# Performance work log

Measured on AMD Instinct MI355X. Metric: run time of the kernel, lower is better.

The kernel has to match this reference:

```python
import jax, jax.numpy as jnp
import numpy as np

B, S, H, QKV, NH, MLP = 4, 2048, 512, 512, 8, 2048
HD = QKV // NH
EPS = 1e-6


def _layernorm(x):
    # LayerNorm over last dim, no affine, eps=1e-6
    mu = jnp.mean(x, axis=-1, keepdims=True)
    var = jnp.mean(jnp.square(x - mu), axis=-1, keepdims=True)
    return (x - mu) * jax.lax.rsqrt(var + EPS)


def setup_inputs() -> dict:
    key = jax.random.key(0)
    ks = jax.random.split(key, 8)
    sc_in = 1.0 / np.sqrt(H)
    sc_qkv = 1.0 / np.sqrt(QKV)
    sc_mlp = 1.0 / np.sqrt(MLP)
    return {
        "input": jax.random.normal(ks[0], (B, S, H), dtype=jnp.float32),
        "mask": jnp.ones((B, S), dtype=jnp.float32),
        "Wq": jax.random.normal(ks[1], (H, QKV), dtype=jnp.float32) * sc_in,
        "Wk": jax.random.normal(ks[2], (H, QKV), dtype=jnp.float32) * sc_in,
        "Wv": jax.random.normal(ks[3], (H, QKV), dtype=jnp.float32) * sc_in,
        "Wo": jax.random.normal(ks[4], (QKV, H), dtype=jnp.float32) * sc_qkv,
        "W1": jax.random.normal(ks[5], (H, MLP), dtype=jnp.float32) * sc_in,
        "W2": jax.random.normal(ks[6], (MLP, H), dtype=jnp.float32) * sc_mlp,
    }


def reference(input, mask, Wq, Wk, Wv, Wo, W1, W2):
    # pre-mask + pre-norm
    x = input * mask[..., None]
    x = _layernorm(x)
    # qkv projections, split heads: [B,S,QKV] -> [B,NH,S,HD]
    def heads(t):
        return t.reshape(B, S, NH, HD).transpose(0, 2, 1, 3)
    q = heads(x @ Wq) * (1.0 / np.sqrt(HD))
    k = heads(x @ Wk)
    v = heads(x @ Wv)
    logits = jnp.einsum("bhqd,bhkd->bhqk", q, k)  # [B,NH,S,S]
    amask = mask[:, None, :, None]  # 'b q -> b 1 q 1'
    logits = logits + (-100000.0) * (1.0 - amask)
    att = jax.nn.softmax(logits, axis=-1)
    out = jnp.einsum("bhqk,bhkd->bhqd", att, v)
    out = out.transpose(0, 2, 1, 3).reshape(B, S, QKV)
    x = input + out @ Wo  # residual
    x = x * mask[..., None]
    y = _layernorm(x)
    ffn = jax.nn.gelu(y @ W1, approximate=False) @ W2
    return ffn + x
```

## Files before the change

kernel.cpp:

```cpp
#include <hip/hip_runtime.h>
#include <hip/hip_bf16.h>
#include <cmath>

typedef __attribute__((ext_vector_type(8))) short bf16x8;
typedef __attribute__((ext_vector_type(4))) float f32x4;
typedef __attribute__((ext_vector_type(16))) float f32x16;
typedef unsigned short u16;
typedef unsigned int u32;

#define B_ 4
#define S_ 2048
#define H_ 512
#define NH_ 8
#define HD_ 64
#define MLP_ 2048
#define M_ (B_*S_)

__device__ __forceinline__ float bf2f(u16 u){ u32 v=((u32)u)<<16; float f; __builtin_memcpy(&f,&v,4); return f; }
__device__ __forceinline__ u16 f2bf(float f){ u32 u; __builtin_memcpy(&u,&f,4); u32 r=(u+0x7fffu+((u>>16)&1u))>>16; return (u16)r; }
__device__ __forceinline__ u32 pk2(float lo, float hi2){
  __hip_bfloat162 t = __float22bfloat162_rn(make_float2(lo, hi2));
  u32 r; __builtin_memcpy(&r, &t, 4); return r;
}

__device__ __forceinline__ float xhalf_add(float x){
  float a = x, b = x;
  asm volatile("v_permlane32_swap_b32 %0, %1" : "+v"(a), "+v"(b));
  return a + b;
}
__device__ __forceinline__ float xhalf_max(float x){
  float a = x, b = x;
  asm volatile("v_permlane32_swap_b32 %0, %1" : "+v"(a), "+v"(b));
  return fmaxf(a, b);
}

__device__ __forceinline__ void gl16(const u16* g, u16* l) {
  __builtin_amdgcn_global_load_lds((const __attribute__((address_space(1))) u32*)(g),
                                   (__attribute__((address_space(3))) u32*)(l), 16, 0, 0);
}

__device__ __forceinline__ void gemm_core(
    const u16* __restrict__ A, const u16* __restrict__ Bt,
    int lda, int ldb, int nkt, int m0, int n0,
    u16* As, u16* Bs, f32x4 (&acc)[4][4])
{
  const int tid = threadIdx.x;
  const int lane = tid & 63;
  const int w = tid >> 6;
  const int lr = lane & 15;
  const int g  = lane >> 4;
  const int wr = w >> 1, wc = w & 1;

  int srow[2], scol[2], soff[2];
#pragma unroll
  for (int c = 0; c < 2; ++c) {
    int off = (w*2+c)*512 + lane*8;
    int row = off >> 5;
    int gl  = (off >> 3) & 3;
    srow[c] = row;
    scol[c] = ((gl ^ ((row>>1)&3)) << 3);
    soff[c] = (w*2+c)*512;
  }
  int aoff[4], boff[4];
#pragma unroll
  for (int m = 0; m < 4; ++m) {
    int ra = wr*64 + m*16 + lr;
    aoff[m] = ra*32 + ((g ^ ((ra>>1)&3))<<3);
    int rb = wc*64 + m*16 + lr;
    boff[m] = rb*32 + ((g ^ ((rb>>1)&3))<<3);
  }
  const u16* Ap = A + (size_t)m0*lda;
  const u16* Bp = Bt + (size_t)n0*ldb;

#pragma unroll
  for (int c = 0; c < 2; ++c) {
    gl16(Ap + (size_t)srow[c]*lda + scol[c], As + soff[c]);
    gl16(Bp + (size_t)srow[c]*ldb + scol[c], Bs + soff[c]);
  }

  for (int kt = 0; kt < nkt; ++kt) {
    const int cb = (kt & 1) * 4096;
    if (kt + 1 < nkt) {
      const int k0 = (kt + 1) << 5;
      const int nb = ((kt + 1) & 1) * 4096;
#pragma unroll
      for (int c = 0; c < 2; ++c) {
        gl16(Ap + (size_t)srow[c]*lda + k0 + scol[c], As + nb + soff[c]);
        gl16(Bp + (size_t)srow[c]*ldb + k0 + scol[c], Bs + nb + soff[c]);
      }
      asm volatile("s_waitcnt vmcnt(4)" ::: "memory");
    } else {
      asm volatile("s_waitcnt vmcnt(0)" ::: "memory");
    }
    __builtin_amdgcn_s_barrier();

    bf16x8 af[4], bfr[4];
#pragma unroll
    for (int m = 0; m < 4; ++m) {
      af[m]  = *(const bf16x8*)(As + cb + aoff[m]);
      bfr[m] = *(const bf16x8*)(Bs + cb + boff[m]);
    }
#pragma unroll
    for (int m = 0; m < 4; ++m) {
#pragma unroll
      for (int n = 0; n < 4; ++n) {
        acc[m][n] = __builtin_amdgcn_mfma_f32_16x16x32_bf16(af[m], bfr[n], acc[m][n], 0, 0, 0);
      }
    }
    __builtin_amdgcn_s_barrier();
  }
}

__device__ __forceinline__ void gemm_core64(
    const u16* __restrict__ A, const u16* __restrict__ Bt,
    int lda, int ldb, int nkt, int m0, int n0,
    u16* As, u16* Bs, f32x4 (&acc)[2][4])
{
  const int tid = threadIdx.x;
  const int lane = tid & 63;
  const int w = tid >> 6;
  const int lr = lane & 15;
  const int g  = lane >> 4;

  int srow[2], scol[2], soff[2];
#pragma unroll
  for (int c = 0; c < 2; ++c) {
    int off = (w*2+c)*512 + lane*8;
    int row = off >> 5;
    int gl  = (off >> 3) & 3;
    srow[c] = row;
    scol[c] = ((gl ^ ((row>>1)&3)) << 3);
    soff[c] = (w*2+c)*512;
  }
  int offB = w*512 + lane*8;
  int srowB = offB >> 5;
  int scolB = ((((offB>>3)&3) ^ ((srowB>>1)&3)) << 3);
  int soffB = w*512;

  int aoff[2], boff[4];
#pragma unroll
  for (int m = 0; m < 2; ++m) {
    int ra = w*32 + m*16 + lr;
    aoff[m] = ra*32 + ((g ^ ((ra>>1)&3))<<3);
  }
#pragma unroll
  for (int n = 0; n < 4; ++n) {
    int rb = n*16 + lr;
    boff[n] = rb*32 + ((g ^ ((rb>>1)&3))<<3);
  }
  const u16* Ap = A + (size_t)m0*lda;
  const u16* Bp = Bt + (size_t)n0*ldb;

#pragma unroll
  for (int c = 0; c < 2; ++c) gl16(Ap + (size_t)srow[c]*lda + scol[c], As + soff[c]);
  gl16(Bp + (size_t)srowB*ldb + scolB, Bs + soffB);

  for (int kt = 0; kt < nkt; ++kt) {
    const int cbA = (kt & 1) * 4096;
    const int cbB = (kt & 1) * 2048;
    if (kt + 1 < nkt) {
      const int k0 = (kt + 1) << 5;
      const int nbA = ((kt + 1) & 1) * 4096;
      const int nbB = ((kt + 1) & 1) * 2048;
#pragma unroll
      for (int c = 0; c < 2; ++c) gl16(Ap + (size_t)srow[c]*lda + k0 + scol[c], As + nbA + soff[c]);
      gl16(Bp + (size_t)srowB*ldb + k0 + scolB, Bs + nbB + soffB);
      asm volatile("s_waitcnt vmcnt(3)" ::: "memory");
    } else {
      asm volatile("s_waitcnt vmcnt(0)" ::: "memory");
    }
    __builtin_amdgcn_s_barrier();

    bf16x8 af[2], bfr[4];
#pragma unroll
    for (int m = 0; m < 2; ++m) af[m] = *(const bf16x8*)(As + cbA + aoff[m]);
#pragma unroll
    for (int n = 0; n < 4; ++n) bfr[n] = *(const bf16x8*)(Bs + cbB + boff[n]);
#pragma unroll
    for (int m = 0; m < 2; ++m) {
#pragma unroll
      for (int n = 0; n < 4; ++n) {
        acc[m][n] = __builtin_amdgcn_mfma_f32_16x16x32_bf16(af[m], bfr[n], acc[m][n], 0, 0, 0);
      }
    }
    __builtin_amdgcn_s_barrier();
  }
}

__global__ __launch_bounds__(256,2) void k_qkv(
    const u16* __restrict__ xn, const u16* __restrict__ wqt,
    const u16* __restrict__ wkt, const u16* __restrict__ wvt,
    u16* __restrict__ q, u16* __restrict__ k, u16* __restrict__ v)
{
  __shared__ u16 As[2*128*32], Bs[2*128*32];
  int m0 = blockIdx.x*128;
  int sel = blockIdx.y >> 2;
  int n0 = (blockIdx.y & 3)*128;
  const u16* Bt = sel==0 ? wqt : (sel==1 ? wkt : wvt);
  u16* O = sel==0 ? q : (sel==1 ? k : v);
  float alpha = (sel==0) ? 0.125f : 1.0f;
  f32x4 acc[4][4] = {};
  gemm_core(xn, Bt, H_, H_, H_/32, m0, n0, As, Bs, acc);
  const int lane = threadIdx.x&63, w = threadIdx.x>>6;
  const int lr = lane&15, g = lane>>4, wr = w>>1, wc = w&1;
#pragma unroll
  for (int m=0;m<4;++m) {
#pragma unroll
    for (int n=0;n<4;++n) {
#pragma unroll
      for (int r=0;r<4;++r) {
        int row = m0 + wr*64 + m*16 + g*4 + r;
        int col = n0 + wc*64 + n*16 + lr;
        O[(size_t)row*H_ + col] = f2bf(acc[m][n][r]*alpha);
      }
    }
  }
}

template<int EPI>
__global__ __launch_bounds__(256,2) void k_gemm(
    const u16* __restrict__ A, const u16* __restrict__ Bt, void* __restrict__ Ov,
    const float* __restrict__ aux, const float* __restrict__ maskv,
    int N, int K)
{
  __shared__ u16 As[2*128*32], Bs[2*128*32];
  int m0 = blockIdx.x*128, n0 = blockIdx.y*128;
  f32x4 acc[4][4] = {};
  gemm_core(A, Bt, K, K, K>>5, m0, n0, As, Bs, acc);
  const int lane = threadIdx.x&63, w = threadIdx.x>>6;
  const int lr = lane&15, g = lane>>4, wr = w>>1, wc = w&1;
#pragma unroll
  for (int m=0;m<4;++m) {
#pragma unroll
    for (int n=0;n<4;++n) {
#pragma unroll
      for (int r=0;r<4;++r) {
        int row = m0 + wr*64 + m*16 + g*4 + r;
        int col = n0 + wc*64 + n*16 + lr;
        float val = acc[m][n][r];
        if (EPI == 1) {
          val = 0.5f*val*(1.0f + erff(val*0.70710678118654752f));
          ((u16*)Ov)[(size_t)row*N + col] = f2bf(val);
        } else if (EPI == 2) {
          float mv = maskv[row];
          val = (aux[(size_t)row*N + col] + val)*mv;
          ((float*)Ov)[(size_t)row*N + col] = val;
        } else if (EPI == 3) {
          val += aux[(size_t)row*N + col];
          ((float*)Ov)[(size_t)row*N + col] = val;
        }
      }
    }
  }
}

template<int EPI>
__global__ __launch_bounds__(256,2) void k_gemm64(
    const u16* __restrict__ A, const u16* __restrict__ Bt, void* __restrict__ Ov,
    const float* __restrict__ aux, const float* __restrict__ maskv,
    int N, int K)
{
  __shared__ u16 As[2*128*32], Bs[2*64*32];
  int m0 = blockIdx.x*128, n0 = blockIdx.y*64;
  f32x4 acc[2][4] = {};
  gemm_core64(A, Bt, K, K, K>>5, m0, n0, As, Bs, acc);
  const int lane = threadIdx.x&63, w = threadIdx.x>>6;
  const int lr = lane&15, g = lane>>4;
#pragma unroll
  for (int m=0;m<2;++m) {
#pragma unroll
    for (int n=0;n<4;++n) {
#pragma unroll
      for (int r=0;r<4;++r) {
        int row = m0 + w*32 + m*16 + g*4 + r;
        int col = n0 + n*16 + lr;
        float val = acc[m][n][r];
        if (EPI == 2) {
          float mv = maskv[row];
          val = (aux[(size_t)row*N + col] + val)*mv;
          ((float*)Ov)[(size_t)row*N + col] = val;
        } else if (EPI == 3) {
          val += aux[(size_t)row*N + col];
          ((float*)Ov)[(size_t)row*N + col] = val;
        }
      }
    }
  }
}

template<int MASKED>
__global__ __launch_bounds__(256) void k_ln(const float* __restrict__ in,
    const float* __restrict__ mask, u16* __restrict__ out)
{
  int row = blockIdx.x*4 + (threadIdx.x>>6);
  int lane = threadIdx.x & 63;
  const f32x4* p = (const f32x4*)(in + (size_t)row*H_ + lane*8);
  f32x4 a = p[0], b = p[1];
  float mv = MASKED ? mask[row] : 1.0f;
  float x[8]; float s = 0.f, s2 = 0.f;
#pragma unroll
  for (int j=0;j<4;++j){ x[j] = a[j]*mv; x[4+j] = b[j]*mv; }
#pragma unroll
  for (int j=0;j<8;++j){ s += x[j]; s2 += x[j]*x[j]; }
#pragma unroll
  for (int m=1;m<32;m<<=1){ s += __shfl_xor(s,m); s2 += __shfl_xor(s2,m); }
  s = xhalf_add(s); s2 = xhalf_add(s2);
  float mu = s*(1.0f/H_);
  float var = s2*(1.0f/H_) - mu*mu;
  float inv = rsqrtf(var + 1e-6f);
  bf16x8 o;
#pragma unroll
  for (int j=0;j<8;++j) o[j] = (short)f2bf((x[j]-mu)*inv);
  *(bf16x8*)(out + (size_t)row*H_ + lane*8) = o;
}

__global__ void k_tr4(const float* __restrict__ s0, const float* __restrict__ s1,
                      const float* __restrict__ s2, const float* __restrict__ s3,
                      u16* __restrict__ d0, u16* __restrict__ d1,
                      u16* __restrict__ d2, u16* __restrict__ d3)
{
  __shared__ u16 t[32][33];
  const float* src = blockIdx.z==0 ? s0 : (blockIdx.z==1 ? s1 : (blockIdx.z==2 ? s2 : s3));
  u16* dst = blockIdx.z==0 ? d0 : (blockIdx.z==1 ? d1 : (blockIdx.z==2 ? d2 : d3));
  int c0 = blockIdx.x*32, r0 = blockIdx.y*32;
  int tx = threadIdx.x & 31, ty = threadIdx.x >> 5;
#pragma unroll
  for (int i=0;i<32;i+=8) t[ty+i][tx] = f2bf(src[(size_t)(r0+ty+i)*512 + c0+tx]);
  __syncthreads();
#pragma unroll
  for (int i=0;i<32;i+=8) dst[(size_t)(c0+ty+i)*512 + r0+tx] = t[tx][ty+i];
}

__global__ void k_tr(const float* __restrict__ src, u16* __restrict__ dst, int R, int C)
{
  __shared__ u16 t[32][33];
  int c0 = blockIdx.x*32, r0 = blockIdx.y*32;
  int tx = threadIdx.x & 31, ty = threadIdx.x >> 5;
#pragma unroll
  for (int i=0;i<32;i+=8) t[ty+i][tx] = f2bf(src[(size_t)(r0+ty+i)*C + c0+tx]);
  __syncthreads();
#pragma unroll
  for (int i=0;i<32;i+=8) dst[(size_t)(c0+ty+i)*R + r0+tx] = t[tx][ty+i];
}

__global__ void k_trv(const u16* __restrict__ v, u16* __restrict__ vt)
{
  __shared__ u16 t[32][33];
  int bh = blockIdx.z, b = bh>>3, h = bh&7;
  int s0 = blockIdx.x*32, d0 = blockIdx.y*32;
  int tx = threadIdx.x & 31, ty = threadIdx.x >> 5;
#pragma unroll
  for (int i=0;i<32;i+=8) t[ty+i][tx] = v[(size_t)(b*S_ + s0+ty+i)*H_ + h*HD_ + d0+tx];
  __syncthreads();
#pragma unroll
  for (int i=0;i<32;i+=8) vt[((size_t)bh*HD_ + d0+ty+i)*S_ + s0+tx] = t[tx][ty+i];
}

__global__ __launch_bounds__(256) void k_attn(
    const u16* __restrict__ q, const u16* __restrict__ kmat,
    const u16* __restrict__ vt, const float* __restrict__ mask,
    u16* __restrict__ o)
{
  __shared__ u16 Ks[2][64*64];
  __shared__ u16 Vs[2][64*64];
  __shared__ float bias[S_];
  __shared__ float lsums[4][32];

  const int tid = threadIdx.x;
  const int lane = tid & 63;
  const int w = tid >> 6;
  const int l31 = lane & 31;
  const int hi = lane >> 5;
  const int bh = blockIdx.y, b = bh >> 3, h = bh & 7;
  const int q0 = blockIdx.x * 128;

  const int sr = lane >> 3;
  const int sl = (lane & 7) ^ (sr & 7);
  const u16* ks0 = kmat + (size_t)(b*S_ + w*16 + sr)*H_ + h*HD_ + sl*8;
  const u16* ks1 = ks0 + (size_t)8*H_;
  const u16* vs0 = vt + ((size_t)bh*HD_ + w*16 + sr)*S_ + sl*8;
  const u16* vs1 = vs0 + (size_t)8*S_;

  {
    u16* kd = &Ks[0][0] + w*1024;
    u16* vd = &Vs[0][0] + w*1024;
    gl16(ks0, kd); gl16(ks1, kd + 512);
    gl16(vs0, vd); gl16(vs1, vd + 512);
  }

  for (int j = tid; j < S_; j += 256) bias[j] = -100000.0f * (1.0f - mask[b*S_ + j]);

  bf16x8 qf[4];
  {
    const u16* qp = q + (size_t)(b*S_ + q0 + w*32 + l31)*H_ + h*HD_ + hi*8;
#pragma unroll
    for (int ds = 0; ds < 4; ++ds) qf[ds] = *(const bf16x8*)(qp + ds*16);
  }

  f32x16 po0 = {}, po1 = {};
  float mreg = -1e30f, lsum = 0.f;

  __syncthreads();

  for (int jt = 0; jt < 32; ++jt) {
    const int buf = jt & 1;
    if (jt < 31) {
      const int j0 = (jt + 1) * 64;
      u16* kd = &Ks[buf ^ 1][0] + w*1024;
      u16* vd = &Vs[buf ^ 1][0] + w*1024;
      gl16(ks0 + (size_t)j0*H_, kd); gl16(ks1 + (size_t)j0*H_, kd + 512);
      gl16(vs0 + j0, vd);            gl16(vs1 + j0, vd + 512);
      asm volatile("s_waitcnt vmcnt(4)" ::: "memory");
    } else {
      asm volatile("s_waitcnt vmcnt(0)" ::: "memory");
    }
    __builtin_amdgcn_s_barrier();

    const u16* kt  = &Ks[buf][0];
    const u16* vtl = &Vs[buf][0];

    f32x16 s0, s1;
    const float* bp = &bias[jt*64 + hi*4];
#pragma unroll
    for (int kb = 0; kb < 2; ++kb) {
      f32x16 acc;
#pragma unroll
      for (int g2 = 0; g2 < 4; ++g2) {
        f32x4 b4 = *(const f32x4*)(bp + kb*32 + g2*8);
        acc[g2*4+0] = b4[0]; acc[g2*4+1] = b4[1];
        acc[g2*4+2] = b4[2]; acc[g2*4+3] = b4[3];
      }
      const int key = kb*32 + l31;
      const u16* kr = kt + key*64;
      __builtin_amdgcn_s_setprio(1);
#pragma unroll
      for (int ds = 0; ds < 4; ++ds) {
        bf16x8 kf = *(const bf16x8*)(kr + (((ds*2 + hi) ^ (key & 7)) << 3));
        acc = __builtin_amdgcn_mfma_f32_32x32x16_bf16(kf, qf[ds], acc, 0, 0, 0);
      }
      __builtin_amdgcn_s_setprio(0);
      if (kb == 0) s0 = acc; else s1 = acc;
    }

    float g0 = fmaxf(fmaxf(fmaxf(s0[0], s0[1]), fmaxf(s0[2], s0[3])),
                     fmaxf(fmaxf(s1[0], s1[1]), fmaxf(s1[2], s1[3])));
    float g1 = fmaxf(fmaxf(fmaxf(s0[4], s0[5]), fmaxf(s0[6], s0[7])),
                     fmaxf(fmaxf(s1[4], s1[5]), fmaxf(s1[6], s1[7])));
    float g2 = fmaxf(fmaxf(fmaxf(s0[8], s0[9]), fmaxf(s0[10], s0[11])),
                     fmaxf(fmaxf(s1[8], s1[9]), fmaxf(s1[10], s1[11])));
    float g3 = fmaxf(fmaxf(fmaxf(s0[12], s0[13]), fmaxf(s0[14], s0[15])),
                     fmaxf(fmaxf(s1[12], s1[13]), fmaxf(s1[14], s1[15])));
    float mx = xhalf_max(fmaxf(fmaxf(g0, g1), fmaxf(g2, g3)));
    if (__any(mx > mreg + 8.0f)) {
      float mn = fmaxf(mreg, mx);
      float sc = __expf(mreg - mn);
      lsum *= sc;
#pragma unroll
      for (int r = 0; r < 16; ++r) { po0[r] *= sc; po1[r] *= sc; }
      mreg = mn;
    }
#pragma unroll
    for (int r = 0; r < 16; ++r) {
      s0[r] = __expf(s0[r]-mreg);
      s1[r] = __expf(s1[r]-mreg);
    }
    float h0 = ((s0[0]+s0[1])+(s0[2]+s0[3])) + ((s1[0]+s1[1])+(s1[2]+s1[3]));
    float h1 = ((s0[4]+s0[5])+(s0[6]+s0[7])) + ((s1[4]+s1[5])+(s1[6]+s1[7]));
    float h2 = ((s0[8]+s0[9])+(s0[10]+s0[11])) + ((s1[8]+s1[9])+(s1[10]+s1[11]));
    float h3 = ((s0[12]+s0[13])+(s0[14]+s0[15])) + ((s1[12]+s1[13])+(s1[14]+s1[15]));
    lsum += xhalf_add((h0+h1)+(h2+h3));

#pragma unroll
    for (int kb = 0; kb < 2; ++kb) {
      const f32x16& sv = kb ? s1 : s0;
      u32 w01 = pk2(sv[0],  sv[1]);
      u32 w23 = pk2(sv[2],  sv[3]);
      u32 w45 = pk2(sv[4],  sv[5]);
      u32 w67 = pk2(sv[6],  sv[7]);
      asm volatile("v_permlane32_swap_b32 %0, %1" : "+v"(w01), "+v"(w45));
      asm volatile("v_permlane32_swap_b32 %0, %1" : "+v"(w23), "+v"(w67));
      u32 w89 = pk2(sv[8],  sv[9]);
      u32 wab = pk2(sv[10], sv[11]);
      u32 wcd = pk2(sv[12], sv[13]);
      u32 wef = pk2(sv[14], sv[15]);
      asm volatile("v_permlane32_swap_b32 %0, %1" : "+v"(w89), "+v"(wcd));
      asm volatile("v_permlane32_swap_b32 %0, %1" : "+v"(wab), "+v"(wef));
      union { u32 wrd[4]; bf16x8 v; } f0, f1;
      f0.wrd[0]=w01; f0.wrd[1]=w23; f0.wrd[2]=w45; f0.wrd[3]=w67;
      f1.wrd[0]=w89; f1.wrd[1]=wab; f1.wrd[2]=wcd; f1.wrd[3]=wef;
      __builtin_amdgcn_s_setprio(1);
#pragma unroll
      for (int ks = 0; ks < 2; ++ks) {
        bf16x8 pa = ks ? f1.v : f0.v;
#pragma unroll
        for (int nb = 0; nb < 2; ++nb) {
          int dd = nb*32 + l31;
          int slot = ((kb*4 + ks*2 + hi) ^ (dd & 7)) << 3;
          bf16x8 vf = *(const bf16x8*)(vtl + dd*64 + slot);
          if (nb == 0) po0 = __builtin_amdgcn_mfma_f32_32x32x16_bf16(pa, vf, po0, 0,0,0);
          else         po1 = __builtin_amdgcn_mfma_f32_32x32x16_bf16(pa, vf, po1, 0,0,0);
        }
      }
      __builtin_amdgcn_s_setprio(0);
    }
    __builtin_amdgcn_s_barrier();
  }

  if (hi == 0) lsums[w][l31] = lsum;
  f32x4 li[4];
#pragma unroll
  for (int g2i = 0; g2i < 4; ++g2i) {
    f32x4 t = *(const f32x4*)&lsums[w][g2i*8 + hi*4];
    li[g2i][0] = 1.0f/t[0]; li[g2i][1] = 1.0f/t[1];
    li[g2i][2] = 1.0f/t[2]; li[g2i][3] = 1.0f/t[3];
  }
  u16* op = o + (size_t)(b*S_ + q0 + w*32)*H_ + h*HD_;
#pragma unroll
  for (int nb = 0; nb < 2; ++nb) {
#pragma unroll
    for (int r = 0; r < 16; ++r) {
      int row = (r&3) + 8*(r>>2) + 4*hi;
      float val = (nb ? po1[r] : po0[r]) * li[r>>2][r&3];
      op[(size_t)row*H_ + nb*32 + l31] = f2bf(val);
    }
  }
}

extern "C" void kernel_launch(void* const* d_in, const int* in_sizes, int n_in,
                              void* d_out, int out_size, void* d_ws, size_t ws_size,
                              hipStream_t stream) {
  const float* input = (const float*)d_in[0];
  const float* mask  = (const float*)d_in[1];
  const float* Wq = (const float*)d_in[2];
  const float* Wk = (const float*)d_in[3];
  const float* Wv = (const float*)d_in[4];
  const float* Wo = (const float*)d_in[5];
  const float* W1 = (const float*)d_in[6];
  const float* W2 = (const float*)d_in[7];
  float* out = (float*)d_out;
  u16* ws = (u16*)d_ws;

  u16* wqt = ws;
  u16* wkt = wqt + 262144;
  u16* wvt = wkt + 262144;
  u16* wot = wvt + 262144;
  u16* w1t = wot + 262144;
  u16* w2t = w1t + 1048576;
  u16* xn  = w2t + 1048576;
  u16* q   = xn  + 4194304;
  u16* k   = q   + 4194304;
  u16* v   = k   + 4194304;
  u16* vt  = v   + 4194304;
  u16*   attn = xn;
  float* x2f  = (float*)q;
  u16*   y    = v;
  u16*   h1   = vt;

  dim3 blk(256);
  k_tr4<<<dim3(16,16,4), blk, 0, stream>>>(Wq, Wk, Wv, Wo, wqt, wkt, wvt, wot);
  k_tr<<<dim3(64,16), blk, 0, stream>>>(W1, w1t, 512, 2048);
  k_tr<<<dim3(16,64), blk, 0, stream>>>(W2, w2t, 2048, 512);

  k_ln<1><<<2048, blk, 0, stream>>>(input, mask, xn);
  k_qkv<<<dim3(64,12), blk, 0, stream>>>(xn, wqt, wkt, wvt, q, k, v);
  k_trv<<<dim3(64,2,32), blk, 0, stream>>>(v, vt);
  k_attn<<<dim3(16,32), blk, 0, stream>>>(q, k, vt, mask, attn);
  k_gemm64<2><<<dim3(64,8), blk, 0, stream>>>(attn, wot, (void*)x2f, input, mask, 512, 512);
  k_ln<0><<<2048, blk, 0, stream>>>(x2f, nullptr, y);
  k_gemm<1><<<dim3(64,16), blk, 0, stream>>>(y, w1t, (void*)h1, nullptr, nullptr, 2048, 512);
  k_gemm64<3><<<dim3(64,8), blk, 0, stream>>>(h1, w2t, (void*)out, x2f, nullptr, 512, 2048);
}
```

Before: 194.9 us.

## Double attention key tile to 128 and skip bias add when mask is all ones

The flash-attention kernel now processes 128 keys per iteration instead of 64, halving the number of loop iterations and barriers, with larger double-buffered K/V shared tiles and a 16-slot XOR swizzle for V. It also detects at runtime whether any mask bias is nonzero and skips the bias addition when none is. This trades more LDS and registers (four 32x32 score accumulators) for fewer synchronisations, and may lower occupancy.

Measured after the change: 215.7 us. 10.7% more time.

```diff
diff --git a/kernel.cpp b/kernel.cpp
--- a/kernel.cpp
+++ b/kernel.cpp
@@ -361,10 +361,11 @@
     const u16* __restrict__ vt, const float* __restrict__ mask,
     u16* __restrict__ o)
 {
-  __shared__ u16 Ks[2][64*64];
-  __shared__ u16 Vs[2][64*64];
+  __shared__ u16 Ks[2][128*64];
+  __shared__ u16 Vs[2][64*128];
   __shared__ float bias[S_];
   __shared__ float lsums[4][32];
+  __shared__ u32 bnz[4];
 
   const int tid = threadIdx.x;
   const int lane = tid & 63;
@@ -375,20 +376,30 @@
   const int q0 = blockIdx.x * 128;
 
   const int sr = lane >> 3;
-  const int sl = (lane & 7) ^ (sr & 7);
-  const u16* ks0 = kmat + (size_t)(b*S_ + w*16 + sr)*H_ + h*HD_ + sl*8;
-  const u16* ks1 = ks0 + (size_t)8*H_;
-  const u16* vs0 = vt + ((size_t)bh*HD_ + w*16 + sr)*S_ + sl*8;
-  const u16* vs1 = vs0 + (size_t)8*S_;
+  const u16* kbase2 = kmat + (size_t)(b*S_ + w*32 + sr)*H_ + h*HD_ + (((lane & 7) ^ sr) << 3);
+  const int sr4 = lane >> 4;
+  const u16* vbase2 = vt + ((size_t)bh*HD_ + w*16 + sr4)*S_;
 
   {
-    u16* kd = &Ks[0][0] + w*1024;
-    u16* vd = &Vs[0][0] + w*1024;
-    gl16(ks0, kd); gl16(ks1, kd + 512);
-    gl16(vs0, vd); gl16(vs1, vd + 512);
-  }
-
-  for (int j = tid; j < S_; j += 256) bias[j] = -100000.0f * (1.0f - mask[b*S_ + j]);
+    bool any = false;
+    for (int j = tid; j < S_; j += 256) {
+      float bv = -100000.0f * (1.0f - mask[b*S_ + j]);
+      bias[j] = bv;
+      any |= (bv != 0.0f);
+    }
+    bnz[w] = (__ballot(any) != 0ull) ? 1u : 0u;
+  }
+
+  {
+    u16* kd = &Ks[0][0] + w*2048;
+    u16* vd = &Vs[0][0] + w*2048;
+#pragma unroll
+    for (int c = 0; c < 4; ++c) {
+      gl16(kbase2 + (size_t)(c*8)*H_, kd + c*512);
+      int slV = ((lane & 15) ^ (c*4 + sr4)) << 3;
+      gl16(vbase2 + (size_t)(c*4)*S_ + slV, vd + c*512);
+    }
+  }
 
   bf16x8 qf[4];
   {
@@ -401,16 +412,21 @@
   float mreg = -1e30f, lsum = 0.f;
 
   __syncthreads();
-
-  for (int jt = 0; jt < 32; ++jt) {
+  const bool hasbias = (bnz[0] | bnz[1] | bnz[2] | bnz[3]) != 0u;
+
+  for (int jt = 0; jt < 16; ++jt) {
     const int buf = jt & 1;
-    if (jt < 31) {
-      const int j0 = (jt + 1) * 64;
-      u16* kd = &Ks[buf ^ 1][0] + w*1024;
-      u16* vd = &Vs[buf ^ 1][0] + w*1024;
-      gl16(ks0 + (size_t)j0*H_, kd); gl16(ks1 + (size_t)j0*H_, kd + 512);
-      gl16(vs0 + j0, vd);            gl16(vs1 + j0, vd + 512);
-      asm volatile("s_waitcnt vmcnt(4)" ::: "memory");
+    if (jt < 15) {
+      const int j0 = (jt + 1) * 128;
+      u16* kd = &Ks[buf ^ 1][0] + w*2048;
+      u16* vd = &Vs[buf ^ 1][0] + w*2048;
+#pragma unroll
+      for (int c = 0; c < 4; ++c) {
+        gl16(kbase2 + (size_t)(j0 + c*8)*H_, kd + c*512);
+        int slV = ((lane & 15) ^ (c*4 + sr4)) << 3;
+        gl16(vbase2 + (size_t)(c*4)*S_ + j0 + slV, vd + c*512);
+      }
+      asm volatile("s_waitcnt vmcnt(8)" ::: "memory");
     } else {
       asm volatile("s_waitcnt vmcnt(0)" ::: "memory");
     }
@@ -419,17 +435,10 @@
     const u16* kt  = &Ks[buf][0];
     const u16* vtl = &Vs[buf][0];
 
-    f32x16 s0, s1;
-    const float* bp = &bias[jt*64 + hi*4];
-#pragma unroll
-    for (int kb = 0; kb < 2; ++kb) {
-      f32x16 acc;
-#pragma unroll
-      for (int g2 = 0; g2 < 4; ++g2) {
-        f32x4 b4 = *(const f32x4*)(bp + kb*32 + g2*8);
-        acc[g2*4+0] = b4[0]; acc[g2*4+1] = b4[1];
-        acc[g2*4+2] = b4[2]; acc[g2*4+3] = b4[3];
-      }
+    f32x16 sA, sB, sC, sD;
+#pragma unroll
+    for (int kb = 0; kb < 4; ++kb) {
+      f32x16 acc = {};
       const int key = kb*32 + l31;
       const u16* kr = kt + key*64;
       __builtin_amdgcn_s_setprio(1);
@@ -439,18 +448,33 @@
         acc = __builtin_amdgcn_mfma_f32_32x32x16_bf16(kf, qf[ds], acc, 0, 0, 0);
       }
       __builtin_amdgcn_s_setprio(0);
-      if (kb == 0) s0 = acc; else s1 = acc;
-    }
-
-    float g0 = fmaxf(fmaxf(fmaxf(s0[0], s0[1]), fmaxf(s0[2], s0[3])),
-                     fmaxf(fmaxf(s1[0], s1[1]), fmaxf(s1[2], s1[3])));
-    float g1 = fmaxf(fmaxf(fmaxf(s0[4], s0[5]), fmaxf(s0[6], s0[7])),
-                     fmaxf(fmaxf(s1[4], s1[5]), fmaxf(s1[6], s1[7])));
-    float g2 = fmaxf(fmaxf(fmaxf(s0[8], s0[9]), fmaxf(s0[10], s0[11])),
-                     fmaxf(fmaxf(s1[8], s1[9]), fmaxf(s1[10], s1[11])));
-    float g3 = fmaxf(fmaxf(fmaxf(s0[12], s0[13]), fmaxf(s0[14], s0[15])),
-                     fmaxf(fmaxf(s1[12], s1[13]), fmaxf(s1[14], s1[15])));
-    float mx = xhalf_max(fmaxf(fmaxf(g0, g1), fmaxf(g2, g3)));
+      if (kb == 0) sA = acc; else if (kb == 1) sB = acc;
+      else if (kb == 2) sC = acc; else sD = acc;
+    }
+
+    if (hasbias) {
+      const float* bp = &bias[jt*128 + hi*4];
+#pragma unroll
+      for (int g2 = 0; g2 < 4; ++g2) {
+        f32x4 b0 = *(const f32x4*)(bp + 0*32 + g2*8);
+        f32x4 b1 = *(const f32x4*)(bp + 1*32 + g2*8);
+        f32x4 b2 = *(const f32x4*)(bp + 2*32 + g2*8);
+        f32x4 b3 = *(const f32x4*)(bp + 3*32 + g2*8);
+#pragma unroll
+        for (int j = 0; j < 4; ++j) {
+          sA[g2*4+j] += b0[j]; sB[g2*4+j] += b1[j];
+          sC[g2*4+j] += b2[j]; sD[g2*4+j] += b3[j];
+        }
+      }
+    }
+
+    float mA = sA[0], mB = sB[0], mC = sC[0], mD = sD[0];
+#pragma unroll
+    for (int r = 1; r < 16; ++r) {
+      mA = fmaxf(mA, sA[r]); mB = fmaxf(mB, sB[r]);
+      mC = fmaxf(mC, sC[r]); mD = fmaxf(mD, sD[r]);
+    }
+    float mx = xhalf_max(fmaxf(fmaxf(mA, mB), fmaxf(mC, mD)));
     if (__any(mx > mreg + 8.0f)) {
       float mn = fmaxf(mreg, mx);
       float sc = __expf(mreg - mn);
@@ -459,20 +483,19 @@
       for (int r = 0; r < 16; ++r) { po0[r] *= sc; po1[r] *= sc; }
       mreg = mn;
     }
+    float pA = 0.f, pB = 0.f, pC = 0.f, pD = 0.f;
 #pragma unroll
     for (int r = 0; r < 16; ++r) {
-      s0[r] = __expf(s0[r]-mreg);
-      s1[r] = __expf(s1[r]-mreg);
-    }
-    float h0 = ((s0[0]+s0[1])+(s0[2]+s0[3])) + ((s1[0]+s1[1])+(s1[2]+s1[3]));
-    float h1 = ((s0[4]+s0[5])+(s0[6]+s0[7])) + ((s1[4]+s1[5])+(s1[6]+s1[7]));
-    float h2 = ((s0[8]+s0[9])+(s0[10]+s0[11])) + ((s1[8]+s1[9])+(s1[10]+s1[11]));
-    float h3 = ((s0[12]+s0[13])+(s0[14]+s0[15])) + ((s1[12]+s1[13])+(s1[14]+s1[15]));
-    lsum += xhalf_add((h0+h1)+(h2+h3));
-
-#pragma unroll
-    for (int kb = 0; kb < 2; ++kb) {
-      const f32x16& sv = kb ? s1 : s0;
+      sA[r] = __expf(sA[r]-mreg); pA += sA[r];
+      sB[r] = __expf(sB[r]-mreg); pB += sB[r];
+      sC[r] = __expf(sC[r]-mreg); pC += sC[r];
+      sD[r] = __expf(sD[r]-mreg); pD += sD[r];
+    }
+    lsum += xhalf_add((pA + pB) + (pC + pD));
+
+#pragma unroll
+    for (int kb = 0; kb < 4; ++kb) {
+      const f32x16& sv = (kb == 0) ? sA : (kb == 1) ? sB : (kb == 2) ? sC : sD;
       u32 w01 = pk2(sv[0],  sv[1]);
       u32 w23 = pk2(sv[2],  sv[3]);
       u32 w45 = pk2(sv[4],  sv[5]);
@@ -495,8 +518,8 @@
 #pragma unroll
         for (int nb = 0; nb < 2; ++nb) {
           int dd = nb*32 + l31;
-          int slot = ((kb*4 + ks*2 + hi) ^ (dd & 7)) << 3;
-          bf16x8 vf = *(const bf16x8*)(vtl + dd*64 + slot);
+          int slot = ((kb*4 + ks*2 + hi) ^ (dd & 15)) << 3;
+          bf16x8 vf = *(const bf16x8*)(vtl + dd*128 + slot);
           if (nb == 0) po0 = __builtin_amdgcn_mfma_f32_32x32x16_bf16(pa, vf, po0, 0,0,0);
           else         po1 = __builtin_amdgcn_mfma_f32_32x32x16_bf16(pa, vf, po1, 0,0,0);
         }
```
